# Optimization experiments

Measured on AMD Instinct MI355X. Metric: run time of the kernel, lower is better.

The kernel has to match this reference:

```python
import jax, jax.numpy as jnp
import numpy as np

D_MODEL = 768
MLP_DIM = 3072
N_EXPERTS = 8
TOP_K = 2
GROUP_DET = 1024
GROUP_CLS = 128


def _route(x, wr, k, capacity):
    """Deterministic top-k softmax router with capacity (vmoe-style).

    x: [G, S, d], wr: [d, E]. Returns dispatch [G,S,E,C] (0/1) and
    combine [G,S,E,C] (gate-weighted).
    """
    G, S, _ = x.shape
    E = wr.shape[1]
    gates = jax.nn.softmax(jnp.einsum('gsd,de->gse', x, wr))  # [G,S,E]
    gval, gidx = jax.lax.top_k(gates, k)                      # [G,S,k]
    # rank-major ordering: all rank-0 choices first, then rank-1, ...
    idx = jnp.swapaxes(gidx, 1, 2).reshape(G, k * S)          # [G,kS]
    val = jnp.swapaxes(gval, 1, 2).reshape(G, k * S)
    oh = jax.nn.one_hot(idx, E, dtype=x.dtype)                # [G,kS,E]
    # position of each assignment in its expert's buffer
    pos = jnp.take_along_axis(jnp.cumsum(oh, axis=1), idx[..., None], axis=2)[..., 0] - 1.0
    keep = (pos < capacity).astype(x.dtype)                   # drop overflow tokens
    posc = jnp.where(pos < capacity, pos, 0.0).astype(jnp.int32)
    slot = jax.nn.one_hot(posc, capacity, dtype=x.dtype)      # [G,kS,C]
    disp = oh[:, :, :, None] * slot[:, :, None, :] * keep[:, :, None, None]  # [G,kS,E,C]
    disp = disp.reshape(G, k, S, E, capacity)
    combine = (disp * val.reshape(G, k, S, 1, 1)).sum(axis=1)  # [G,S,E,C]
    dispatch = disp.sum(axis=1)                                # [G,S,E,C]
    return dispatch, combine


def _expert_mlp(xe, w1, b1, w2, b2):
    # xe: [E,G,C,d]; per-expert params w1:[E,d,m], b1:[E,m], w2:[E,m,d], b2:[E,d]
    h = jax.nn.gelu(jnp.einsum('egcd,edm->egcm', xe, w1) + b1[:, None, None, :])
    return jnp.einsum('egcm,emd->egcd', h, w2) + b2[:, None, None, :]


def _moe_stream(x3, group_size, wr, w1, b1, w2, b2):
    B, S, d = x3.shape
    x = x3.reshape(-1, group_size, d)                         # [G,gs,d]
    capacity = group_size * TOP_K // N_EXPERTS
    dispatch, combine = _route(x, wr, TOP_K, capacity)
    xe = jnp.einsum('gsec,gsd->egcd', dispatch, x)            # gather to experts
    ye = _expert_mlp(xe, w1, b1, w2, b2)                      # grouped MLP
    y = jnp.einsum('gsec,egcd->gsd', combine, ye)             # weighted scatter back
    return y.reshape(B, S, d)


def setup_inputs() -> dict:
    key = jax.random.key(0)
    ks = jax.random.split(key, 8)
    xav1 = float(np.sqrt(6.0 / (D_MODEL + MLP_DIM)))
    xavr = float(np.sqrt(6.0 / (D_MODEL + N_EXPERTS)))
    return {
        'inputs_det': jax.random.normal(ks[0], (8, 1024, D_MODEL), jnp.float32),
        'inputs_cls': jax.random.normal(ks[1], (8, 128, D_MODEL), jnp.float32),
        'wr_det': jax.random.uniform(ks[2], (D_MODEL, N_EXPERTS), jnp.float32, -xavr, xavr),
        'wr_cls': jax.random.uniform(ks[3], (D_MODEL, N_EXPERTS), jnp.float32, -xavr, xavr),
        'w1': jax.random.uniform(ks[4], (N_EXPERTS, D_MODEL, MLP_DIM), jnp.float32, -xav1, xav1),
        'b1': jax.random.normal(ks[5], (N_EXPERTS, MLP_DIM), jnp.float32) * 1e-6,
        'w2': jax.random.uniform(ks[6], (N_EXPERTS, MLP_DIM, D_MODEL), jnp.float32, -xav1, xav1),
        'b2': jax.random.normal(ks[7], (N_EXPERTS, D_MODEL), jnp.float32) * 1e-6,
    }


def reference(inputs_det, inputs_cls, wr_det, wr_cls, w1, b1, w2, b2):
    out_det = _moe_stream(inputs_det, GROUP_DET, wr_det, w1, b1, w2, b2)
    out_cls = _moe_stream(inputs_cls, GROUP_CLS, wr_cls, w1, b1, w2, b2)
    return (out_det, out_cls)
```

## Files before the change

kernel.cpp:

```cpp
#include <hip/hip_runtime.h>
#include <hip/hip_bf16.h>
#include <math.h>

typedef __bf16 bf16;
typedef __bf16 bf16x8 __attribute__((ext_vector_type(8)));
typedef __bf16 bf16x4 __attribute__((ext_vector_type(4)));
typedef float  f32x4  __attribute__((ext_vector_type(4)));

#define D_MODEL 768
#define MLP_DIM 3072

#define SZ_W1T   ((size_t)8*3072*768*2)
#define SZ_W2T   ((size_t)8*768*3072*2)
#define SZ_XED   ((size_t)8*8*256*768*2)
#define SZ_XEC   ((size_t)8*8*32*768*2)
#define SZ_HD    ((size_t)8*2048*3072*2)
#define SZ_HC    ((size_t)8*256*3072*2)
#define SZ_YED   ((size_t)8*2048*768*2)
#define SZ_YEC   ((size_t)8*256*768*2)
#define SZ_RID   ((size_t)8192*8)
#define SZ_RGD   ((size_t)8192*8)
#define SZ_RIC   ((size_t)1024*8)
#define SZ_RGC   ((size_t)1024*8)
#define SZ_STD   ((size_t)8*8*256*4)
#define SZ_STC   ((size_t)8*8*32*4)
#define SZ_TSD   ((size_t)2*8192*4)
#define SZ_TSC   ((size_t)2*1024*4)

#define OFF_W1T  ((size_t)0)
#define OFF_W2T  (OFF_W1T + SZ_W1T)
#define OFF_XED  (OFF_W2T + SZ_W2T)
#define OFF_XEC  (OFF_XED + SZ_XED)
#define OFF_HD   (OFF_XEC + SZ_XEC)
#define OFF_HC   (OFF_HD  + SZ_HD)
#define OFF_YED  (OFF_HC  + SZ_HC)
#define OFF_YEC  (OFF_YED + SZ_YED)
#define OFF_RID  (OFF_YEC + SZ_YEC)
#define OFF_RGD  (OFF_RID + SZ_RID)
#define OFF_RIC  (OFF_RGD + SZ_RGD)
#define OFF_RGC  (OFF_RIC + SZ_RIC)
#define OFF_STD  (OFF_RGC + SZ_RGC)
#define OFF_STC  (OFF_STD + SZ_STD)
#define OFF_TSD  (OFF_STC + SZ_STC)
#define OFF_TSC  (OFF_TSD + SZ_TSD)

__device__ __forceinline__ void lds_load16(const void* g, void* l) {
  __builtin_amdgcn_global_load_lds((__attribute__((address_space(1))) void*)g,
                                   (__attribute__((address_space(3))) void*)l,
                                   16, 0, 0);
}

__device__ __forceinline__ float gelu_fast(float x) {
  float x2 = x * x;
  float z = x * __builtin_fmaf(-0.07135481627f, x2, -1.5957691216f);
  float e = __expf(z);
  return x * __builtin_amdgcn_rcpf(1.f + e);
}

__global__ void convt_router_kernel(const float* __restrict__ w1, bf16* __restrict__ w1t,
                                    const float* __restrict__ w2, bf16* __restrict__ w2t,
                                    const float* __restrict__ xd, const float* __restrict__ wrd,
                                    const float* __restrict__ xc, const float* __restrict__ wrc,
                                    int2* __restrict__ rid, float2* __restrict__ rgd,
                                    int2* __restrict__ ric, float2* __restrict__ rgc) {
  int bid = blockIdx.x;
  if (bid < 2304) {
    const float *x, *wr; int2* ridx; float2* rgate;
    if (bid < 2048) { x = xd; wr = wrd; ridx = rid; rgate = rgd; }
    else { bid -= 2048; x = xc; wr = wrc; ridx = ric; rgate = rgc; }
    int wave = threadIdx.x >> 6;
    int lane = threadIdx.x & 63;
    int t = bid * 4 + wave;
    const float* xr = x + (size_t)t * D_MODEL;
    float acc[8];
#pragma unroll
    for (int e = 0; e < 8; ++e) acc[e] = 0.f;
    for (int d = lane; d < D_MODEL; d += 64) {
      float xv = xr[d];
      const float* w = wr + d * 8;
      float4 a = *(const float4*)w;
      float4 b = *(const float4*)(w + 4);
      acc[0] += xv * a.x; acc[1] += xv * a.y; acc[2] += xv * a.z; acc[3] += xv * a.w;
      acc[4] += xv * b.x; acc[5] += xv * b.y; acc[6] += xv * b.z; acc[7] += xv * b.w;
    }
#pragma unroll
    for (int off = 32; off > 0; off >>= 1) {
#pragma unroll
      for (int e = 0; e < 8; ++e) acc[e] += __shfl_xor(acc[e], off, 64);
    }
    float mx = acc[0];
#pragma unroll
    for (int e = 1; e < 8; ++e) mx = fmaxf(mx, acc[e]);
    float p[8]; float z = 0.f;
#pragma unroll
    for (int e = 0; e < 8; ++e) { p[e] = __expf(acc[e] - mx); z += p[e]; }
    int i1 = 0;
#pragma unroll
    for (int e = 1; e < 8; ++e) if (p[e] > p[i1]) i1 = e;
    int i2 = (i1 == 0) ? 1 : 0;
#pragma unroll
    for (int e = 0; e < 8; ++e) if (e != i1 && p[e] > p[i2]) i2 = e;
    if (lane == 0) {
      float inv = 1.f / z;
      ridx[t]  = make_int2(i1, i2);
      rgate[t] = make_float2(p[i1] * inv, p[i2] * inv);
    }
    return;
  }
  bid -= 2304;
  __shared__ float tile[64][65];
  const float* src; bf16* dst; int K, N;
  if (bid < 4608) { src = w1; dst = w1t; K = 768; N = 3072; }
  else { bid -= 4608; src = w2; dst = w2t; K = 3072; N = 768; }
  int e = bid / 576;
  int t = bid - e * 576;
  int tiles_x = N >> 6;
  int ky = t / tiles_x;
  int n0 = (t - ky * tiles_x) * 64, k0 = ky * 64;
  const float* S_ = src + (size_t)e * K * N;
  bf16* D_ = dst + (size_t)e * K * N;
  int tx = threadIdx.x & 15, ty = threadIdx.x >> 4;
#pragma unroll
  for (int i = 0; i < 4; ++i) {
    float4 v = *(const float4*)(S_ + (size_t)(k0 + ty + i * 16) * N + (n0 + tx * 4));
    int r = ty + i * 16, c = tx * 4;
    tile[r][c] = v.x; tile[r][c + 1] = v.y; tile[r][c + 2] = v.z; tile[r][c + 3] = v.w;
  }
  __syncthreads();
  int n = threadIdx.x >> 2, kq = (threadIdx.x & 3) * 16;
  bf16 o[16];
#pragma unroll
  for (int j = 0; j < 16; ++j) o[j] = (bf16)tile[kq + j][n];
  bf16* drow = D_ + (size_t)(n0 + n) * K + (k0 + kq);
  *(bf16x8*)drow       = *(const bf16x8*)o;
  *(bf16x8*)(drow + 8) = *(const bf16x8*)(o + 8);
}

__global__ void positions_kernel(const int2* __restrict__ rid, int* __restrict__ std_,
                                 int* __restrict__ tsd_, const int2* __restrict__ ric,
                                 int* __restrict__ stc_, int* __restrict__ tsc_) {
  __shared__ int2 sh[1024];
  int bid = blockIdx.x;
  const int2* ridx; int *slot_token, *tok_slot; int S, C, g;
  if (bid < 8) { ridx = rid; slot_token = std_; tok_slot = tsd_; S = 1024; C = 256; g = bid; }
  else { ridx = ric; slot_token = stc_; tok_slot = tsc_; S = 128; C = 32; g = bid - 8; }
  int lane = threadIdx.x;
  int ntok = 8 * S;
  for (int i = lane; i < S; i += 64) sh[i] = ridx[g * S + i];
  __builtin_amdgcn_s_waitcnt(0);
  unsigned long long ltmask = (1ull << lane) - 1ull;
  int cnt[8];
#pragma unroll
  for (int e = 0; e < 8; ++e) cnt[e] = 0;
  int nch = (2 * S) >> 6;
  for (int ch = 0; ch < nch; ++ch) {
    int a = (ch << 6) + lane;
    int r = (a >= S) ? 1 : 0;
    int s = a - r * S;
    int2 id = sh[s];
    int  e  = r ? id.y : id.x;
    unsigned long long mymask = 0;
    int add[8];
#pragma unroll
    for (int ee = 0; ee < 8; ++ee) {
      unsigned long long mk = __ballot(e == ee);
      if (e == ee) mymask = mk;
      add[ee] = __popcll(mk);
    }
    int pos = cnt[e] + __popcll(mymask & ltmask);
    int sl = (e * 8 + g) * C + pos;
    if (pos < C) slot_token[sl] = s;
    tok_slot[r * ntok + g * S + s] = (pos < C) ? sl : -1;
#pragma unroll
    for (int ee = 0; ee < 8; ++ee) cnt[ee] += add[ee];
  }
#pragma unroll
  for (int e = 0; e < 8; ++e) {
    for (int i = cnt[e] + lane; i < C; i += 64)
      slot_token[(e * 8 + g) * C + i] = -1;
  }
}

__global__ void gather_kernel(const float* __restrict__ xd, const int* __restrict__ std_,
                              bf16* __restrict__ xed, const float* __restrict__ xc,
                              const int* __restrict__ stc_, bf16* __restrict__ xec,
                              int splitd) {
  int bid = blockIdx.x;
  const float* x; const int* slot_token; bf16* xe; int S, C;
  if (bid < splitd) { x = xd; slot_token = std_; xe = xed; S = 1024; C = 256; }
  else { bid -= splitd; x = xc; slot_token = stc_; xe = xec; S = 128; C = 32; }
  int slot = bid * 4 + (threadIdx.x >> 6);
  int lane = threadIdx.x & 63;
  int g = (slot / C) & 7;
  int s = slot_token[slot];
  bf16* dst = xe + (size_t)slot * D_MODEL;
  const float* xr = x + ((size_t)g * S + (s < 0 ? 0 : s)) * D_MODEL;
#pragma unroll
  for (int j = 0; j < 3; ++j) {
    int idx = j * 256 + lane * 4;
    float4 v;
    if (s >= 0) v = *(const float4*)(xr + idx);
    else        v = make_float4(0.f, 0.f, 0.f, 0.f);
    bf16 o[4] = {(bf16)v.x, (bf16)v.y, (bf16)v.z, (bf16)v.w};
    *(uint2*)(dst + idx) = *(const uint2*)o;
  }
}

__global__ void combine_kernel(const int* __restrict__ tsd_, const float2* __restrict__ rgd,
                               const bf16* __restrict__ yed, float* __restrict__ outd,
                               const int* __restrict__ tsc_, const float2* __restrict__ rgc,
                               const bf16* __restrict__ yec, float* __restrict__ outc,
                               int splitd) {
  int bid = blockIdx.x;
  const int* tok_slot; const float2* rgate; const bf16* ye; float* out; int ntok;
  if (bid < splitd) { tok_slot = tsd_; rgate = rgd; ye = yed; out = outd; ntok = 8192; }
  else { bid -= splitd; tok_slot = tsc_; rgate = rgc; ye = yec; out = outc; ntok = 1024; }
  int t = bid * 4 + (threadIdx.x >> 6);
  int lane = threadIdx.x & 63;
  int s1 = tok_slot[t];
  int s2 = tok_slot[ntok + t];
  float2 gg = rgate[t];
  float g1 = (s1 < 0) ? 0.f : gg.x;
  float g2 = (s2 < 0) ? 0.f : gg.y;
  const bf16* y1 = ye + (size_t)(s1 < 0 ? 0 : s1) * D_MODEL;
  const bf16* y2 = ye + (size_t)(s2 < 0 ? 0 : s2) * D_MODEL;
  float* orow = out + (size_t)t * D_MODEL;
#pragma unroll
  for (int j = 0; j < 3; ++j) {
    int idx = j * 256 + lane * 4;
    bf16x4 a = *(const bf16x4*)(y1 + idx);
    bf16x4 b = *(const bf16x4*)(y2 + idx);
    float4 o;
    o.x = g1 * (float)a[0] + g2 * (float)b[0];
    o.y = g1 * (float)a[1] + g2 * (float)b[1];
    o.z = g1 * (float)a[2] + g2 * (float)b[2];
    o.w = g1 * (float)a[3] + g2 * (float)b[3];
    *(float4*)(orow + idx) = o;
  }
}

template <int GELU>
__launch_bounds__(256, 3)
__global__ void gemm_mfma(const bf16* __restrict__ Adet, const bf16* __restrict__ Acls,
                          const bf16* __restrict__ Btall, const float* __restrict__ biasall,
                          int Mdet, int Mcls, int N, int K,
                          int Nmd, int Nmc, int Nn, int minner, int splitd,
                          bf16* __restrict__ Odet, bf16* __restrict__ Ocls) {
  int bid = blockIdx.x;
  const bf16* Aall; bf16* Oall; int M, Nm;
  if (bid < splitd) { Aall = Adet; Oall = Odet; M = Mdet; Nm = Nmd; }
  else { bid -= splitd; Aall = Acls; Oall = Ocls; M = Mcls; Nm = Nmc; }
  const int e   = bid & 7;
  const int seq = bid >> 3;
  int m_t, n_t;
  if (minner) { n_t = seq / Nm; m_t = seq - n_t * Nm; }
  else        { m_t = seq / Nn; n_t = seq - m_t * Nn; }
  const int n0 = n_t * 128;
  const int m0 = m_t * 128;
  const int tid  = threadIdx.x;
  const int wave = tid >> 6, lane = tid & 63;
  const int wm = (wave >> 1) * 64, wn = (wave & 1) * 64;
  const int lrow = lane & 15, lquad = lane >> 4;

  __shared__ __align__(16) bf16 smem[16384];
  bf16* As = smem;
  bf16* Bs = smem + 8192;

  const bf16* A  = Aall  + (size_t)e * M * K;
  const bf16* Bt = Btall + (size_t)e * N * K;

  const int srow = tid >> 3;
  const int gq   = (tid & 7) ^ (srow & 7);
  const bf16* Asrc = A  + (size_t)(m0 + srow) * K + gq * 8;
  const bf16* Bsrc = Bt + (size_t)(n0 + srow) * K + gq * 8;
  char* AsB = (char*)As;
  char* BsB = (char*)Bs;
  const int ldsw = wave * 1024;

  const float* bias = biasall + (size_t)e * N;
  float bfr[4];
#pragma unroll
  for (int ni = 0; ni < 4; ++ni) bfr[ni] = bias[n0 + wn + ni * 16 + lrow];

  f32x4 acc[4][4];
#pragma unroll
  for (int mi = 0; mi < 4; ++mi)
#pragma unroll
    for (int ni = 0; ni < 4; ++ni) acc[mi][ni] = {0.f, 0.f, 0.f, 0.f};

  const int xsw = lrow & 7;
  const int nsteps = K >> 6;
  for (int kt = 0; kt < nsteps; ++kt) {
    const bf16* a0 = Asrc + kt * 64;
    const bf16* b0 = Bsrc + kt * 64;
#pragma unroll
    for (int rd = 0; rd < 4; ++rd) {
      lds_load16(a0 + (size_t)(rd * 32) * K, AsB + rd * 4096 + ldsw);
      lds_load16(b0 + (size_t)(rd * 32) * K, BsB + rd * 4096 + ldsw);
    }
    __syncthreads();
#pragma unroll
    for (int h = 0; h < 2; ++h) {
      bf16x8 fa[4], fb[4];
      const int ca = ((h * 4 + lquad) ^ xsw) * 8;
#pragma unroll
      for (int i = 0; i < 4; ++i) {
        fa[i] = *(const bf16x8*)(As + (wm + i * 16 + lrow) * 64 + ca);
        fb[i] = *(const bf16x8*)(Bs + (wn + i * 16 + lrow) * 64 + ca);
      }
#pragma unroll
      for (int mi = 0; mi < 4; ++mi)
#pragma unroll
        for (int ni = 0; ni < 4; ++ni)
          acc[mi][ni] = __builtin_amdgcn_mfma_f32_16x16x32_bf16(fa[mi], fb[ni], acc[mi][ni], 0, 0, 0);
    }
    __syncthreads();
  }

#pragma unroll
  for (int mi = 0; mi < 4; ++mi) {
#pragma unroll
    for (int r = 0; r < 4; ++r) {
      int row = wm + mi * 16 + lquad * 4 + r;
#pragma unroll
      for (int ni = 0; ni < 4; ++ni) {
        int colL = wn + ni * 16 + lrow;
        float v = acc[mi][ni][r] + bfr[ni];
        if (GELU) v = gelu_fast(v);
        int chunk = (colL >> 3) ^ (row & 7);
        smem[row * 128 + chunk * 8 + (colL & 7)] = (bf16)v;
      }
    }
  }
  __syncthreads();
  bf16* O = Oall + (size_t)e * M * N;
#pragma unroll
  for (int it = 0; it < 8; ++it) {
    int idx = it * 256 + tid;
    int row = idx >> 4;
    int ck  = idx & 15;
    int pchunk = ck ^ (row & 7);
    bf16x8 vv = *(const bf16x8*)(smem + row * 128 + pchunk * 8);
    *(bf16x8*)(O + (size_t)(m0 + row) * N + n0 + ck * 8) = vv;
  }
}

extern "C" void kernel_launch(void* const* d_in, const int* in_sizes, int n_in,
                              void* d_out, int out_size, void* d_ws, size_t ws_size,
                              hipStream_t stream) {
  (void)in_sizes; (void)n_in; (void)ws_size; (void)out_size;
  const float* x_det  = (const float*)d_in[0];
  const float* x_cls  = (const float*)d_in[1];
  const float* wr_det = (const float*)d_in[2];
  const float* wr_cls = (const float*)d_in[3];
  const float* w1     = (const float*)d_in[4];
  const float* b1     = (const float*)d_in[5];
  const float* w2     = (const float*)d_in[6];
  const float* b2     = (const float*)d_in[7];
  float* out = (float*)d_out;
  char*  ws  = (char*)d_ws;

  bf16*   w1t    = (bf16*)(ws + OFF_W1T);
  bf16*   w2t    = (bf16*)(ws + OFF_W2T);
  bf16*   xe_det = (bf16*)(ws + OFF_XED);
  bf16*   xe_cls = (bf16*)(ws + OFF_XEC);
  bf16*   h_det  = (bf16*)(ws + OFF_HD);
  bf16*   h_cls  = (bf16*)(ws + OFF_HC);
  bf16*   ye_det = (bf16*)(ws + OFF_YED);
  bf16*   ye_cls = (bf16*)(ws + OFF_YEC);
  int2*   ri_det = (int2*)(ws + OFF_RID);
  float2* rg_det = (float2*)(ws + OFF_RGD);
  int2*   ri_cls = (int2*)(ws + OFF_RIC);
  float2* rg_cls = (float2*)(ws + OFF_RGC);
  int*    st_det = (int*)(ws + OFF_STD);
  int*    st_cls = (int*)(ws + OFF_STC);
  int*    ts_det = (int*)(ws + OFF_TSD);
  int*    ts_cls = (int*)(ws + OFF_TSC);

  convt_router_kernel<<<2304 + 2 * 4608, 256, 0, stream>>>(
      w1, w1t, w2, w2t, x_det, wr_det, x_cls, wr_cls,
      ri_det, rg_det, ri_cls, rg_cls);

  positions_kernel<<<16, 64, 0, stream>>>(ri_det, st_det, ts_det, ri_cls, st_cls, ts_cls);

  gather_kernel<<<4096 + 512, 256, 0, stream>>>(x_det, st_det, xe_det, x_cls, st_cls, xe_cls, 4096);

  gemm_mfma<1><<<8 * 16 * 24 + 8 * 2 * 24, 256, 0, stream>>>(
      xe_det, xe_cls, w1t, b1, 2048, 256, 3072, 768,
      16, 2, 24, 1, 8 * 16 * 24, h_det, h_cls);

  gemm_mfma<0><<<8 * 16 * 6 + 8 * 2 * 6, 256, 0, stream>>>(
      h_det, h_cls, w2t, b2, 2048, 256, 768, 3072,
      16, 2, 6, 0, 8 * 16 * 6, ye_det, ye_cls);

  combine_kernel<<<2048 + 256, 256, 0, stream>>>(ts_det, rg_det, ye_det, out,
                                                 ts_cls, rg_cls, ye_cls,
                                                 out + (size_t)8192 * 768, 2048);
}
```

Measured before the change: 459.1 us.

## Add 256x256-tile 8-wave ping-pong MFMA GEMM for second expert matmul

Adds a new 512-thread GEMM kernel with 256x256 output tiles, a double-buffered LDS pipeline, interleaved global-to-LDS staging and MFMA phases, and s_setprio scheduling. The second expert GEMM (h x w2) now uses it instead of the 128-tile kernel. The goal is more operand reuse per LDS load and better overlap of memory and compute on the long-K (3072) GEMM. In exchange the grid is much smaller (216 blocks), which may underfill the GPU's compute units, and the kernel uses 128KB of LDS, which limits occupancy.

```diff
diff --git a/kernel.cpp b/kernel.cpp
--- a/kernel.cpp
+++ b/kernel.cpp
@@ -345,6 +345,163 @@
   }
 }
 
+template <int GELU>
+__launch_bounds__(512, 2)
+__global__ void gemm_mfma8p(const bf16* __restrict__ Adet, const bf16* __restrict__ Acls,
+                            const bf16* __restrict__ Btall, const float* __restrict__ biasall,
+                            int Mdet, int Mcls, int N, int K,
+                            int Nmd, int Nmc, int Nn, int minner, int splitd,
+                            bf16* __restrict__ Odet, bf16* __restrict__ Ocls) {
+  int bid = blockIdx.x;
+  const bf16* Aall; bf16* Oall; int M, Nm;
+  if (bid < splitd) { Aall = Adet; Oall = Odet; M = Mdet; Nm = Nmd; }
+  else { bid -= splitd; Aall = Acls; Oall = Ocls; M = Mcls; Nm = Nmc; }
+  const int e   = bid & 7;
+  const int seq = bid >> 3;
+  int m_t, n_t;
+  if (minner) { n_t = seq / Nm; m_t = seq - n_t * Nm; }
+  else        { m_t = seq / Nn; n_t = seq - m_t * Nn; }
+  const int n0 = n_t * 256;
+  const int m0 = m_t * 256;
+  const int tid  = threadIdx.x;
+  const int wave = tid >> 6, lane = tid & 63;
+  const int wm = (wave >> 2) * 128, wn = (wave & 3) * 64;
+  const int lrow = lane & 15, lquad = lane >> 4;
+
+  __shared__ __align__(16) bf16 smem[65536];
+  char* smemB = (char*)smem;
+
+  const bf16* A  = Aall  + (size_t)e * M * K;
+  const bf16* Bt = Btall + (size_t)e * N * K;
+
+  const int srow0 = tid >> 3;
+  const int gq    = (tid & 7) ^ (srow0 & 7);
+  const bf16* Asrc = A  + (size_t)(m0 + srow0) * K + gq * 8;
+  const bf16* Bsrc = Bt + (size_t)(n0 + srow0) * K + gq * 8;
+  const int ldsw = wave * 1024;
+
+  const int aBase = (wm ? 8192 : 0) + lrow * 64;
+  const int bBase = 16384 + (wn >= 128 ? 8192 : 0) + (wn & 64) * 64 + lrow * 64;
+  const int ca0 = (lquad ^ (lrow & 7)) * 8;
+  const int ca1 = ca0 ^ 32;
+
+  const float* bias = biasall + (size_t)e * N;
+  float bfr[4];
+#pragma unroll
+  for (int ni = 0; ni < 4; ++ni) bfr[ni] = bias[n0 + wn + ni * 16 + lrow];
+
+  f32x4 acc[8][4];
+#pragma unroll
+  for (int mi = 0; mi < 8; ++mi)
+#pragma unroll
+    for (int ni = 0; ni < 4; ++ni) acc[mi][ni] = {0.f, 0.f, 0.f, 0.f};
+
+  bf16x8 fa[2][4], fb0[2][2], fb1[2][2];
+
+#define STG_A(buf, half, kt) do { \
+    const bf16* _s = Asrc + (size_t)((half) * 128) * K + (size_t)(kt) * 64; \
+    char* _d = smemB + (buf) * 65536 + (half) * 16384 + ldsw; \
+    lds_load16(_s, _d); \
+    lds_load16(_s + (size_t)64 * K, _d + 8192); \
+  } while (0)
+#define STG_B(buf, half, kt) do { \
+    const bf16* _s = Bsrc + (size_t)((half) * 128) * K + (size_t)(kt) * 64; \
+    char* _d = smemB + (buf) * 65536 + 32768 + (half) * 16384 + ldsw; \
+    lds_load16(_s, _d); \
+    lds_load16(_s + (size_t)64 * K, _d + 8192); \
+  } while (0)
+#define LDA(buf, qm) do { \
+    const bf16* _p = smem + (buf) * 32768 + aBase + (qm) * 4096; \
+    _Pragma("unroll") \
+    for (int _i = 0; _i < 4; ++_i) { \
+      fa[0][_i] = *(const bf16x8*)(_p + _i * 1024 + ca0); \
+      fa[1][_i] = *(const bf16x8*)(_p + _i * 1024 + ca1); \
+    } \
+  } while (0)
+#define LDB(buf, qn, FB) do { \
+    const bf16* _p = smem + (buf) * 32768 + bBase + (qn) * 2048; \
+    _Pragma("unroll") \
+    for (int _j = 0; _j < 2; ++_j) { \
+      FB[0][_j] = *(const bf16x8*)(_p + _j * 1024 + ca0); \
+      FB[1][_j] = *(const bf16x8*)(_p + _j * 1024 + ca1); \
+    } \
+  } while (0)
+#define MM(qm, qn, FB) do { \
+    __builtin_amdgcn_s_setprio(1); \
+    _Pragma("unroll") \
+    for (int _h = 0; _h < 2; ++_h) \
+      _Pragma("unroll") \
+      for (int _i = 0; _i < 4; ++_i) \
+        _Pragma("unroll") \
+        for (int _j = 0; _j < 2; ++_j) \
+          acc[(qm) * 4 + _i][(qn) * 2 + _j] = __builtin_amdgcn_mfma_f32_16x16x32_bf16( \
+              fa[_h][_i], FB[_h][_j], acc[(qm) * 4 + _i][(qn) * 2 + _j], 0, 0, 0); \
+    __builtin_amdgcn_s_setprio(0); \
+  } while (0)
+#define BAR() __builtin_amdgcn_s_barrier()
+#define VMC4() asm volatile("s_waitcnt vmcnt(4)" ::: "memory")
+
+  const int nt = K >> 6;
+  const int niter = nt >> 1;
+
+  STG_B(0, 0, 0); STG_B(0, 1, 0); STG_A(0, 0, 0); STG_A(0, 1, 0);
+  STG_B(1, 0, 1); STG_B(1, 1, 1);
+  VMC4();
+  BAR();
+
+  for (int it = 0; it < niter; ++it) {
+    const int k1 = 2 * it + 1;
+    const int k2 = (2 * it + 2 < nt) ? 2 * it + 2 : nt - 1;
+    const int k3 = (2 * it + 3 < nt) ? 2 * it + 3 : nt - 1;
+    LDA(0, 0); LDB(0, 0, fb0); STG_A(1, 0, k1); BAR(); MM(0, 0, fb0); BAR();
+    LDB(0, 1, fb1);            STG_A(1, 1, k1); BAR(); MM(0, 1, fb1); BAR();
+    LDA(0, 1);                 STG_B(0, 0, k2); BAR(); MM(1, 1, fb1); BAR();
+                               STG_B(0, 1, k2); VMC4();
+                                                BAR(); MM(1, 0, fb0); BAR();
+    LDA(1, 0); LDB(1, 0, fb0); STG_A(0, 0, k2); BAR(); MM(0, 0, fb0); BAR();
+    LDB(1, 1, fb1);            STG_A(0, 1, k2); BAR(); MM(0, 1, fb1); BAR();
+    LDA(1, 1);                 STG_B(1, 0, k3); BAR(); MM(1, 1, fb1); BAR();
+                               STG_B(1, 1, k3); VMC4();
+                                                BAR(); MM(1, 0, fb0); BAR();
+  }
+
+#undef STG_A
+#undef STG_B
+#undef LDA
+#undef LDB
+#undef MM
+#undef BAR
+#undef VMC4
+
+  __syncthreads();
+#pragma unroll
+  for (int mi = 0; mi < 8; ++mi) {
+#pragma unroll
+    for (int r = 0; r < 4; ++r) {
+      int row = wm + mi * 16 + lquad * 4 + r;
+#pragma unroll
+      for (int ni = 0; ni < 4; ++ni) {
+        int colL = wn + ni * 16 + lrow;
+        float v = acc[mi][ni][r] + bfr[ni];
+        if (GELU) v = gelu_fast(v);
+        int chunk = (colL >> 3) ^ (row & 7);
+        smem[row * 256 + chunk * 8 + (colL & 7)] = (bf16)v;
+      }
+    }
+  }
+  __syncthreads();
+  bf16* O = Oall + (size_t)e * M * N;
+#pragma unroll
+  for (int itw = 0; itw < 16; ++itw) {
+    int idx = itw * 512 + tid;
+    int row = idx >> 5;
+    int ck  = idx & 31;
+    int pchunk = ck ^ (row & 7);
+    bf16x8 vv = *(const bf16x8*)(smem + row * 256 + pchunk * 8);
+    *(bf16x8*)(O + (size_t)(m0 + row) * N + n0 + ck * 8) = vv;
+  }
+}
+
 extern "C" void kernel_launch(void* const* d_in, const int* in_sizes, int n_in,
                               void* d_out, int out_size, void* d_ws, size_t ws_size,
                               hipStream_t stream) {
@@ -389,9 +546,9 @@
       xe_det, xe_cls, w1t, b1, 2048, 256, 3072, 768,
       16, 2, 24, 1, 8 * 16 * 24, h_det, h_cls);
 
-  gemm_mfma<0><<<8 * 16 * 6 + 8 * 2 * 6, 256, 0, stream>>>(
+  gemm_mfma8p<0><<<8 * 8 * 3 + 8 * 1 * 3, 512, 0, stream>>>(
       h_det, h_cls, w2t, b2, 2048, 256, 768, 3072,
-      16, 2, 6, 0, 8 * 16 * 6, ye_det, ye_cls);
+      8, 1, 3, 0, 8 * 8 * 3, ye_det, ye_cls);
 
   combine_kernel<<<2048 + 256, 256, 0, stream>>>(ts_det, rg_det, ye_det, out,
                                                  ts_cls, rg_cls, ye_cls,
```

Result: faster. 436.6 us (-4.9%).
